# Kernel optimization log

Measured on AMD Instinct MI355X. Metric: run time of the kernel, lower is better.

Reference implementation:

```python
import jax, jax.numpy as jnp
import numpy as np

K_NEAREST = 5
EPS = 1e-6


def setup_inputs() -> dict:
    key = jax.random.key(0)
    k1, k2, k3 = jax.random.split(key, 3)
    N_Q, N_DB, D_OUT, D_AUX = 4096, 65536, 32, 32
    return {
        "embedding_features": jax.random.normal(k1, (N_Q, D_OUT), dtype=jnp.float32),
        "db_embedding": jax.random.normal(k2, (N_DB, D_OUT), dtype=jnp.float32),
        "auxiliary_features": jax.random.normal(k3, (N_DB, D_AUX), dtype=jnp.float32),
    }


def reference(embedding_features, db_embedding, auxiliary_features):
    d_out = embedding_features.shape[-1]
    q = embedding_features.reshape(-1, d_out)          # [Nq, D]
    db = db_embedding.reshape(-1, d_out)               # [Ndb, D]

    # Euclidean cdist via the expanded quadratic form (same math as torch.cdist p=2).
    q_sq = jnp.sum(q * q, axis=1, keepdims=True)       # [Nq, 1]
    db_sq = jnp.sum(db * db, axis=1)[None, :]          # [1, Ndb]
    dist_sq = q_sq + db_sq - 2.0 * (q @ db.T)          # [Nq, Ndb]
    distances = jnp.sqrt(jnp.maximum(dist_sq, 0.0))

    # k smallest distances == k largest of negated distances.
    neg_top, nearest_indices = jax.lax.top_k(-distances, K_NEAREST)  # [Nq, k]
    nearest_distances = -neg_top                                      # [Nq, k]

    aux = auxiliary_features.reshape(-1, auxiliary_features.shape[-1])
    nearest_aux = aux[nearest_indices]                 # [Nq, k, Daux]

    weights = 1.0 / (nearest_distances + EPS)
    weights = weights / jnp.sum(weights, axis=1, keepdims=True)

    return jnp.sum(nearest_aux * weights[..., None], axis=1)  # [Nq, Daux]
```

## Files before the change

kernel.cpp:

```cpp
#include <hip/hip_runtime.h>
#include <math.h>

#define N_Q   4096
#define N_DB  65536
#define DIM   32
#define KNN   5
#define NC    64
#define CH    (N_DB / NC)
#define TS    128
#define NSTG  (CH / TS)
#define NSUB  (TS / 32)
#define NCAND (NC * 6)
#define BIAS  256.0f

typedef _Float16 half8  __attribute__((ext_vector_type(8)));
typedef __fp16   fp16x2 __attribute__((ext_vector_type(2)));
typedef float floatx16  __attribute__((ext_vector_type(16)));

union H8  { half8 h; uint4 u4; unsigned u[4]; };
union F16 { floatx16 v; float4 q4[4]; unsigned w[16]; };
union HU  { fp16x2 h2; unsigned u; };

__device__ __forceinline__ unsigned cvt2(float a, float b) {
    HU t; t.h2 = __builtin_amdgcn_cvt_pkrtz(a, b);
    return t.u;
}

__device__ __forceinline__ void ld_lds16(const void* g, void* l) {
    __builtin_amdgcn_global_load_lds((const __attribute__((address_space(1))) unsigned*)g,
                                     (__attribute__((address_space(3))) unsigned*)l, 16, 0, 0);
}
__device__ __forceinline__ void ld_lds4(const void* g, void* l) {
    __builtin_amdgcn_global_load_lds((const __attribute__((address_space(1))) unsigned*)g,
                                     (__attribute__((address_space(3))) unsigned*)l, 4, 0, 0);
}

__global__ __launch_bounds__(256) void k_prep(const float* __restrict__ DB,
                                              uint4* __restrict__ DBh,
                                              float* __restrict__ hdb) {
    int p = blockIdx.x * 256 + threadIdx.x;
    const float4* src = (const float4*)(DB + (size_t)p * DIM);
    float4 f[8]; float s = 0.f;
#pragma unroll
    for (int j = 0; j < 8; ++j) {
        f[j] = src[j];
        s += f[j].x * f[j].x + f[j].y * f[j].y + f[j].z * f[j].z + f[j].w * f[j].w;
    }
    hdb[p] = BIAS - 0.5f * s;
    int t = p >> 5, r = p & 31;
#pragma unroll
    for (int gi = 0; gi < 4; ++gi) {
        uint4 g;
        g.x = cvt2(f[2 * gi].x, f[2 * gi].y);
        g.y = cvt2(f[2 * gi].z, f[2 * gi].w);
        g.z = cvt2(f[2 * gi + 1].x, f[2 * gi + 1].y);
        g.w = cvt2(f[2 * gi + 1].z, f[2 * gi + 1].w);
        DBh[(size_t)t * 128 + gi * 32 + r] = g;
    }
}

__global__ __launch_bounds__(256, 6) void k_scan(const float* __restrict__ Q,
                                                 const uint4* __restrict__ DBh,
                                                 const float* __restrict__ hdb,
                                                 unsigned* __restrict__ cand) {
    __shared__ char  dbs[2][8192];
    __shared__ float hbs[2][TS];

    const int tid = threadIdx.x, lane = tid & 63, w = tid >> 6;
    const int h = lane >> 5, qcol = lane & 31;
    const int chunk = blockIdx.x & (NC - 1);
    const int qb    = blockIdx.x >> 6;
    const int q     = qb * 128 + w * 32 + qcol;
    const int pbase = chunk * CH;

    const float* qp = Q + (size_t)q * DIM;
    float4 qa = *(const float4*)(qp + h * 8);
    float4 qb4 = *(const float4*)(qp + h * 8 + 4);
    float4 qc = *(const float4*)(qp + 16 + h * 8);
    float4 qd = *(const float4*)(qp + 16 + h * 8 + 4);
    H8 b1, b2;
    b1.u[0] = cvt2(qa.x, qa.y);   b1.u[1] = cvt2(qa.z, qa.w);
    b1.u[2] = cvt2(qb4.x, qb4.y); b1.u[3] = cvt2(qb4.z, qb4.w);
    b2.u[0] = cvt2(qc.x, qc.y);   b2.u[1] = cvt2(qc.z, qc.w);
    b2.u[2] = cvt2(qd.x, qd.y);   b2.u[3] = cvt2(qd.z, qd.w);

    unsigned maskv;
    asm("v_mov_b32 %0, 0xFFFFFC00" : "=v"(maskv));

    auto stage = [&](int buf, int t) {
        const char* s = (const char*)DBh + (size_t)pbase * 64 + (size_t)t * 8192
                        + w * 1024 + lane * 16;
        char* d = dbs[buf] + w * 1024;
        ld_lds16(s, d);
        ld_lds16(s + 4096, d + 4096);
        if (w < 2)
            ld_lds4(hdb + pbase + t * TS + w * 64 + lane,
                    (char*)&hbs[buf][0] + w * 256);
    };

    float tk[6];
#pragma unroll
    for (int r = 0; r < 6; ++r) tk[r] = 0.f;

    constexpr int ROWC[16] = {0,1,2,3, 8,9,10,11, 16,17,18,19, 24,25,26,27};

    stage(0, 0);
    for (int t = 0; t < NSTG; ++t) {
        __syncthreads();
        if (t + 1 < NSTG) stage((t + 1) & 1, t + 1);
        const int buf = t & 1;
        const char* base = dbs[buf];
#pragma unroll
        for (int sub = 0; sub < NSUB; ++sub) {
            const char* tb = base + sub * 2048;
            H8 a1, a2;
            a1.u4 = *(const uint4*)(tb + h * 512 + (lane & 31) * 16);
            a2.u4 = *(const uint4*)(tb + 1024 + h * 512 + (lane & 31) * 16);
            F16 c0;
            const float* hb = &hbs[buf][sub * 32 + 4 * h];
            c0.q4[0] = *(const float4*)(hb + 0);
            c0.q4[1] = *(const float4*)(hb + 8);
            c0.q4[2] = *(const float4*)(hb + 16);
            c0.q4[3] = *(const float4*)(hb + 24);
            floatx16 acc = __builtin_amdgcn_mfma_f32_32x32x16_f16(a1.h, b1.h, c0.v, 0, 0, 0);
            acc = __builtin_amdgcn_mfma_f32_32x32x16_f16(a2.h, b2.h, acc, 0, 0, 0);
            F16 pk; pk.v = acc;
            const int meta = (t * NSUB + sub) << 5;
            float p[16];
#pragma unroll
            for (int r = 0; r < 16; ++r)
                p[r] = __uint_as_float((pk.w[r] & maskv) | (unsigned)(meta | ROWC[r]));
            float hi[8], lo[8];
#pragma unroll
            for (int i = 0; i < 8; ++i) { hi[i] = fmaxf(p[2*i], p[2*i+1]); lo[i] = fminf(p[2*i], p[2*i+1]); }
            float H4[4], L4[4];
#pragma unroll
            for (int i = 0; i < 4; ++i) {
                H4[i] = fmaxf(hi[2*i], hi[2*i+1]);
                L4[i] = fmaxf(fmaxf(lo[2*i], lo[2*i+1]), fminf(hi[2*i], hi[2*i+1]));
            }
            float H2[2], L2[2];
#pragma unroll
            for (int i = 0; i < 2; ++i) {
                H2[i] = fmaxf(H4[2*i], H4[2*i+1]);
                L2[i] = fmaxf(fmaxf(L4[2*i], L4[2*i+1]), fminf(H4[2*i], H4[2*i+1]));
            }
            float c1 = fmaxf(H2[0], H2[1]);
            float c2 = fmaxf(fmaxf(L2[0], L2[1]), fminf(H2[0], H2[1]));
            {
                float m01 = fminf(tk[0], c1), m02 = fminf(tk[1], c1);
                float m03 = fminf(tk[2], c1), m04 = fminf(tk[3], c1);
                float m05 = fminf(tk[4], c1);
                float m12 = fminf(tk[0], c2), m13 = fminf(tk[1], c2);
                float m14 = fminf(tk[2], c2), m15 = fminf(tk[3], c2);
                tk[0] = fmaxf(tk[0], c1);
                tk[1] = fmaxf(fmaxf(tk[1], m01), c2);
                tk[2] = fmaxf(fmaxf(tk[2], m02), m12);
                tk[3] = fmaxf(fmaxf(tk[3], m03), m13);
                tk[4] = fmaxf(fmaxf(tk[4], m04), m14);
                tk[5] = fmaxf(fmaxf(tk[5], m05), m15);
            }
        }
    }

#pragma unroll
    for (int r = 0; r < 6; ++r)
        tk[r] = __uint_as_float(__float_as_uint(tk[r]) | (unsigned)(h << 2));

    float other[6];
#pragma unroll
    for (int i = 0; i < 6; ++i) other[i] = __shfl_xor(tk[i], 32, 64);
#pragma unroll
    for (int i = 0; i < 6; ++i) {
        float val = other[i];
#pragma unroll
        for (int j = 0; j < 6; ++j) { float mx = fmaxf(tk[j], val); val = fminf(tk[j], val); tk[j] = mx; }
    }
    if (h == 0) {
        unsigned* dst = cand + ((size_t)q * NC + chunk) * 6;
#pragma unroll
        for (int r = 0; r < 6; ++r) dst[r] = __float_as_uint(tk[r]);
    }
}

__global__ __launch_bounds__(256) void k_merge(const float* __restrict__ Q,
                                               const float* __restrict__ DB,
                                               const float* __restrict__ AUX,
                                               const unsigned* __restrict__ cand,
                                               float* __restrict__ out) {
    const int tid = threadIdx.x, lane = tid & 63, w = tid >> 6;
    const int q = blockIdx.x * 4 + w;

    const unsigned* cq = cand + (size_t)q * NCAND + (size_t)lane * 6;
    float cur[6];
#pragma unroll
    for (int r = 0; r < 6; ++r) cur[r] = __uint_as_float(cq[r]);

    float wv[12]; int wl[12];
#pragma unroll
    for (int r = 0; r < 12; ++r) {
        float bv = cur[0]; int bl = lane;
#pragma unroll
        for (int off = 32; off >= 1; off >>= 1) {
            float ov = __shfl_xor(bv, off, 64);
            int   ol = __shfl_xor(bl, off, 64);
            if (ov > bv || (ov == bv && ol < bl)) { bv = ov; bl = ol; }
        }
        wv[r] = bv; wl[r] = bl;
        if (bl == lane) {
#pragma unroll
            for (int s = 0; s < 5; ++s) cur[s] = cur[s + 1];
            cur[5] = -1.f;
        }
    }

    float dist = 1e30f; int dbi = 0x7fffffff;
    if (lane < 12) {
        unsigned u = __float_as_uint(wv[lane]) & 1023u;
        dbi = wl[lane] * CH + (int)u;
        const float4* dp = (const float4*)(DB + (size_t)dbi * DIM);
        const float4* qp = (const float4*)(Q + (size_t)q * DIM);
        float dot = 0.f, qs = 0.f, ds = 0.f;
#pragma unroll
        for (int j = 0; j < DIM / 4; ++j) {
            float4 a = qp[j], d = dp[j];
            dot += a.x * d.x + a.y * d.y + a.z * d.z + a.w * d.w;
            qs  += a.x * a.x + a.y * a.y + a.z * a.z + a.w * a.w;
            ds  += d.x * d.x + d.y * d.y + d.z * d.z + d.w * d.w;
        }
        dist = sqrtf(fmaxf(qs + ds - 2.f * dot, 0.f));
    }
    float wd[KNN]; int wi[KNN];
#pragma unroll
    for (int r = 0; r < KNN; ++r) {
        float bd = dist; int bi = dbi;
#pragma unroll
        for (int off = 32; off >= 1; off >>= 1) {
            float od = __shfl_xor(bd, off, 64);
            int   oi = __shfl_xor(bi, off, 64);
            if (od < bd || (od == bd && oi < bi)) { bd = od; bi = oi; }
        }
        wd[r] = bd; wi[r] = bi;
        if (dist == bd && dbi == bi) dist = 1e30f;
    }
    float ww[KNN], W = 0.f;
#pragma unroll
    for (int r = 0; r < KNN; ++r) { ww[r] = 1.f / (wd[r] + 1e-6f); W += ww[r]; }
    if (lane < DIM) {
        float o = 0.f;
#pragma unroll
        for (int r = 0; r < KNN; ++r) o += ww[r] * AUX[(size_t)wi[r] * DIM + lane];
        out[(size_t)q * DIM + lane] = o / W;
    }
}

extern "C" void kernel_launch(void* const* d_in, const int* in_sizes, int n_in,
                              void* d_out, int out_size, void* d_ws, size_t ws_size,
                              hipStream_t stream) {
    const float* Q   = (const float*)d_in[0];
    const float* DB  = (const float*)d_in[1];
    const float* AUX = (const float*)d_in[2];
    float* out = (float*)d_out;

    char* ws = (char*)d_ws;
    uint4*    DBh = (uint4*)ws;                         ws += (size_t)(N_DB / 32) * 128 * 16;
    float*    hdb = (float*)ws;                         ws += (size_t)N_DB * 4;
    unsigned* cand = (unsigned*)ws;

    k_prep<<<N_DB / 256, 256, 0, stream>>>(DB, DBh, hdb);
    k_scan<<<(N_Q / 128) * NC, 256, 0, stream>>>(Q, DBh, hdb, cand);
    k_merge<<<N_Q / 4, 256, 0, stream>>>(Q, DB, AUX, cand, out);
}
```

Measured before the change: 137.6 us.

## Fold norm bias into a third MFMA and preload chunk norms once

The per-point bias (256 - 0.5*||db||^2) now comes from an extra fp16 MFMA that multiplies a [nb, 1] row by a constant [1, 256] column, instead of building the accumulator init from four float4 LDS reads per subtile. The norms are stored as fp16 and the whole chunk's norms are loaded into LDS once at kernel start rather than per stage. The loop is also unrolled by two with literal buffer indices. This adds a third MFMA per subtile and rounds the norm term to fp16, which may perturb the candidate ordering used by the prefilter.

```diff
diff --git a/kernel.cpp b/kernel.cpp
--- a/kernel.cpp
+++ b/kernel.cpp
@@ -11,7 +11,6 @@
 #define NSTG  (CH / TS)
 #define NSUB  (TS / 32)
 #define NCAND (NC * 6)
-#define BIAS  256.0f
 
 typedef _Float16 half8  __attribute__((ext_vector_type(8)));
 typedef __fp16   fp16x2 __attribute__((ext_vector_type(2)));
@@ -30,14 +29,10 @@
     __builtin_amdgcn_global_load_lds((const __attribute__((address_space(1))) unsigned*)g,
                                      (__attribute__((address_space(3))) unsigned*)l, 16, 0, 0);
 }
-__device__ __forceinline__ void ld_lds4(const void* g, void* l) {
-    __builtin_amdgcn_global_load_lds((const __attribute__((address_space(1))) unsigned*)g,
-                                     (__attribute__((address_space(3))) unsigned*)l, 4, 0, 0);
-}
 
 __global__ __launch_bounds__(256) void k_prep(const float* __restrict__ DB,
                                               uint4* __restrict__ DBh,
-                                              float* __restrict__ hdb) {
+                                              unsigned short* __restrict__ hdbh) {
     int p = blockIdx.x * 256 + threadIdx.x;
     const float4* src = (const float4*)(DB + (size_t)p * DIM);
     float4 f[8]; float s = 0.f;
@@ -46,7 +41,7 @@
         f[j] = src[j];
         s += f[j].x * f[j].x + f[j].y * f[j].y + f[j].z * f[j].z + f[j].w * f[j].w;
     }
-    hdb[p] = BIAS - 0.5f * s;
+    hdbh[p] = (unsigned short)(cvt2(-0.5f * s, 0.f) & 0xFFFFu);
     int t = p >> 5, r = p & 31;
 #pragma unroll
     for (int gi = 0; gi < 4; ++gi) {
@@ -61,17 +56,21 @@
 
 __global__ __launch_bounds__(256, 6) void k_scan(const float* __restrict__ Q,
                                                  const uint4* __restrict__ DBh,
-                                                 const float* __restrict__ hdb,
+                                                 const unsigned short* __restrict__ hdbh,
                                                  unsigned* __restrict__ cand) {
-    __shared__ char  dbs[2][8192];
-    __shared__ float hbs[2][TS];
+    __shared__ char dbs[2][8192];
+    __shared__ unsigned short nh[CH];
 
     const int tid = threadIdx.x, lane = tid & 63, w = tid >> 6;
-    const int h = lane >> 5, qcol = lane & 31;
+    const int h = lane >> 5;
     const int chunk = blockIdx.x & (NC - 1);
     const int qb    = blockIdx.x >> 6;
-    const int q     = qb * 128 + w * 32 + qcol;
+    const int q     = qb * 128 + w * 32 + (lane & 31);
     const int pbase = chunk * CH;
+
+    if (w < 2)
+        ld_lds16((const char*)hdbh + (size_t)pbase * 2 + w * 1024 + lane * 16,
+                 (char*)&nh[0] + w * 1024);
 
     const float* qp = Q + (size_t)q * DIM;
     float4 qa = *(const float4*)(qp + h * 8);
@@ -84,6 +83,10 @@
     b2.u[0] = cvt2(qc.x, qc.y);   b2.u[1] = cvt2(qc.z, qc.w);
     b2.u[2] = cvt2(qd.x, qd.y);   b2.u[3] = cvt2(qd.z, qd.w);
 
+    H8 b3;
+    b3.u[0] = h ? 0u : 0x5C003C00u;
+    b3.u[1] = 0u; b3.u[2] = 0u; b3.u[3] = 0u;
+
     unsigned maskv;
     asm("v_mov_b32 %0, 0xFFFFFC00" : "=v"(maskv));
 
@@ -93,9 +96,6 @@
         char* d = dbs[buf] + w * 1024;
         ld_lds16(s, d);
         ld_lds16(s + 4096, d + 4096);
-        if (w < 2)
-            ld_lds4(hdb + pbase + t * TS + w * 64 + lane,
-                    (char*)&hbs[buf][0] + w * 256);
     };
 
     float tk[6];
@@ -104,26 +104,24 @@
 
     constexpr int ROWC[16] = {0,1,2,3, 8,9,10,11, 16,17,18,19, 24,25,26,27};
 
-    stage(0, 0);
-    for (int t = 0; t < NSTG; ++t) {
-        __syncthreads();
-        if (t + 1 < NSTG) stage((t + 1) & 1, t + 1);
-        const int buf = t & 1;
-        const char* base = dbs[buf];
+    auto process = [&](int bufLit, int t) {
+        const char* base = dbs[bufLit];
 #pragma unroll
         for (int sub = 0; sub < NSUB; ++sub) {
             const char* tb = base + sub * 2048;
             H8 a1, a2;
             a1.u4 = *(const uint4*)(tb + h * 512 + (lane & 31) * 16);
             a2.u4 = *(const uint4*)(tb + 1024 + h * 512 + (lane & 31) * 16);
-            F16 c0;
-            const float* hb = &hbs[buf][sub * 32 + 4 * h];
-            c0.q4[0] = *(const float4*)(hb + 0);
-            c0.q4[1] = *(const float4*)(hb + 8);
-            c0.q4[2] = *(const float4*)(hb + 16);
-            c0.q4[3] = *(const float4*)(hb + 24);
-            floatx16 acc = __builtin_amdgcn_mfma_f32_32x32x16_f16(a1.h, b1.h, c0.v, 0, 0, 0);
+            unsigned nb = (unsigned)nh[(t * NSUB + sub) * 32 + (lane & 31)];
+            unsigned r0 = nb | 0x3C000000u;
+            H8 a3;
+            a3.u[0] = h ? 0u : r0;
+            a3.u[1] = 0u; a3.u[2] = 0u; a3.u[3] = 0u;
+
+            floatx16 acc = __builtin_amdgcn_mfma_f32_32x32x16_f16(a3.h, b3.h, (floatx16)(0.f), 0, 0, 0);
+            acc = __builtin_amdgcn_mfma_f32_32x32x16_f16(a1.h, b1.h, acc, 0, 0, 0);
             acc = __builtin_amdgcn_mfma_f32_32x32x16_f16(a2.h, b2.h, acc, 0, 0, 0);
+
             F16 pk; pk.v = acc;
             const int meta = (t * NSUB + sub) << 5;
             float p[16];
@@ -161,6 +159,16 @@
                 tk[5] = fmaxf(fmaxf(tk[5], m05), m15);
             }
         }
+    };
+
+    stage(0, 0);
+    for (int tt = 0; tt < NSTG; tt += 2) {
+        __syncthreads();
+        if (tt + 1 < NSTG) stage(1, tt + 1);
+        process(0, tt);
+        __syncthreads();
+        if (tt + 2 < NSTG) stage(0, tt + 2);
+        process(1, tt + 1);
     }
 
 #pragma unroll
@@ -263,11 +271,11 @@
     float* out = (float*)d_out;
 
     char* ws = (char*)d_ws;
-    uint4*    DBh = (uint4*)ws;                         ws += (size_t)(N_DB / 32) * 128 * 16;
-    float*    hdb = (float*)ws;                         ws += (size_t)N_DB * 4;
-    unsigned* cand = (unsigned*)ws;
-
-    k_prep<<<N_DB / 256, 256, 0, stream>>>(DB, DBh, hdb);
-    k_scan<<<(N_Q / 128) * NC, 256, 0, stream>>>(Q, DBh, hdb, cand);
+    uint4*          DBh  = (uint4*)ws;                  ws += (size_t)(N_DB / 32) * 128 * 16;
+    unsigned short* hdbh = (unsigned short*)ws;         ws += (size_t)N_DB * 2;
+    unsigned*       cand = (unsigned*)ws;
+
+    k_prep<<<N_DB / 256, 256, 0, stream>>>(DB, DBh, hdbh);
+    k_scan<<<(N_Q / 128) * NC, 256, 0, stream>>>(Q, DBh, hdbh, cand);
     k_merge<<<N_Q / 4, 256, 0, stream>>>(Q, DB, AUX, cand, out);
 }
```

Measured after the change: 158.6 us. +15.3%, slower.
